# Kernel optimization log

Measured on AMD Instinct MI355X. Metric: run time of the kernel, lower is better.

## Reference

```python
import jax, jax.numpy as jnp
import numpy as np

N = 50000
IN_C, HID_C, CLS_C = 512, 256, 128
E = 800000


def setup_inputs() -> dict:
    key = jax.random.key(0)
    k1, k2, k3, k4, k5, k6 = jax.random.split(key, 6)
    x = jax.random.normal(k1, (N, IN_C), dtype=jnp.float32)
    edge_index = jax.random.randint(k2, (2, E), 0, N, dtype=jnp.int64)
    # GCNConv params (glorot weights, zero bias as in PyG init)
    W1 = jax.random.normal(k3, (IN_C, HID_C), dtype=jnp.float32) * (1.0 / np.sqrt(IN_C))
    b1 = jnp.zeros((HID_C,), dtype=jnp.float32)
    W2 = jax.random.normal(k4, (HID_C, CLS_C), dtype=jnp.float32) * (1.0 / np.sqrt(HID_C))
    b2 = jnp.zeros((CLS_C,), dtype=jnp.float32)
    return {"x": x, "W1": W1, "b1": b1, "W2": W2, "b2": b2, "edge_index": edge_index}


def _norm_edges(edge_index, n):
    # PyG GCNConv: add self-loops, symmetric normalization deg^-1/2
    loops = jnp.arange(n, dtype=edge_index.dtype)
    src = jnp.concatenate([edge_index[0], loops])
    dst = jnp.concatenate([edge_index[1], loops])
    ones = jnp.ones_like(src, dtype=jnp.float32)
    deg = jax.ops.segment_sum(ones, dst, num_segments=n)
    dinv = jnp.where(deg > 0, jax.lax.rsqrt(deg), 0.0)
    norm = dinv[src] * dinv[dst]  # [E+N]
    return src, dst, norm


def _gcn_conv(x, W, b, src, dst, norm, n):
    h = x @ W  # project first (out_channels < in_channels)
    msg = h[src] * norm[:, None]  # gather + scale, [E+N, C]
    out = jax.ops.segment_sum(msg, dst, num_segments=n)  # scatter-add
    return out + b


def reference(x, W1, b1, W2, b2, edge_index):
    n = x.shape[0]
    src, dst, norm = _norm_edges(edge_index, n)
    h = jax.nn.relu(_gcn_conv(x, W1, b1, src, dst, norm, n))
    # dropout p=0.5 is a no-op in eval mode
    out = _gcn_conv(h, W2, b2, src, dst, norm, n)
    return jax.nn.sigmoid(out)
```

## Files before the change

### kernel.cpp

```cpp
#include <hip/hip_runtime.h>

typedef __attribute__((ext_vector_type(8))) short bf16x8;
typedef __attribute__((ext_vector_type(4))) float f32x4;
typedef unsigned short u16;
typedef unsigned int u32;
typedef __attribute__((address_space(1))) const u32 gu32;
typedef __attribute__((address_space(3))) u32 lu32;

__device__ __forceinline__ float bf2f(u16 u) {
  union { u32 i; float f; } c; c.i = ((u32)u) << 16; return c.f;
}
__device__ __forceinline__ u16 f2bf(float f) {
  union { float f; u32 i; } c; c.f = f;
  u32 u = c.i;
  u32 r = (u + 0x7FFFu + ((u >> 16) & 1u)) >> 16;
  return (u16)r;
}

__device__ __forceinline__ void gld16(const void* g, void* l) {
  __builtin_amdgcn_global_load_lds((gu32*)g, (lu32*)l, 16, 0, 0);
}


__global__ void k_count(const int* __restrict__ ei, int* deg, int E) {
  int e = blockIdx.x * 256 + threadIdx.x;
  if (e < E) atomicAdd(&deg[ei[E + e]], 1);
}

__global__ void k_blocksum(const int* __restrict__ deg, int* bsum, int n) {
  __shared__ int s[256];
  int t = threadIdx.x;
  int i = blockIdx.x * 256 + t;
  s[t] = (i < n) ? deg[i] : 0;
  __syncthreads();
  for (int o = 128; o > 0; o >>= 1) {
    if (t < o) s[t] += s[t + o];
    __syncthreads();
  }
  if (t == 0) bsum[blockIdx.x] = s[0];
}

__global__ void k_scanb(const int* __restrict__ bsum, int* bofs, int nb) {
  __shared__ int s[256];
  int t = threadIdx.x;
  int v = (t < nb) ? bsum[t] : 0;
  s[t] = v;
  __syncthreads();
  for (int o = 1; o < 256; o <<= 1) {
    int x = (t >= o) ? s[t - o] : 0;
    __syncthreads();
    s[t] += x;
    __syncthreads();
  }
  bofs[t] = s[t] - v;
}

__global__ void k_rowptr(const int* __restrict__ deg, const int* __restrict__ bofs,
                         int* rowptr, int* cursor, float* dinv, int n) {
  __shared__ int s[256];
  int t = threadIdx.x;
  int i = blockIdx.x * 256 + t;
  int v = (i < n) ? deg[i] : 0;
  s[t] = v;
  __syncthreads();
  for (int o = 1; o < 256; o <<= 1) {
    int x = (t >= o) ? s[t - o] : 0;
    __syncthreads();
    s[t] += x;
    __syncthreads();
  }
  int excl = s[t] - v + bofs[blockIdx.x];
  if (i < n) {
    rowptr[i] = excl;
    cursor[i] = excl;
    dinv[i] = rsqrtf((float)(v + 1));
    if (i == n - 1) rowptr[n] = excl + v;
  }
}

__global__ void k_fill(const int* __restrict__ ei, int* cursor,
                       const float* __restrict__ dinv, int2* colw, int E) {
  int e = blockIdx.x * 256 + threadIdx.x;
  if (e >= E) return;
  int s = ei[e];
  int d = ei[E + e];
  int pos = atomicAdd(&cursor[d], 1);
  colw[pos] = make_int2(s, __float_as_int(dinv[s]));
}

__global__ void k_twt2(const float* __restrict__ W1, u16* __restrict__ W1t,
                       const float* __restrict__ W2, u16* __restrict__ W2t) {
  int i = blockIdx.x * 256 + threadIdx.x;
  if (i < 512 * 256) {
    int k = i >> 8, n = i & 255;
    W1t[n * 512 + k] = f2bf(W1[i]);
  } else {
    int j = i - 512 * 256;
    if (j < 256 * 128) {
      int k = j >> 7, n = j & 127;
      W2t[n * 256 + k] = f2bf(W2[j]);
    }
  }
}


template <bool AF32, int K, int BM, int MAXB>
__launch_bounds__(256, MAXB)
__global__ void gemm_kernel(const void* __restrict__ Ap, const u16* __restrict__ Bt,
                            u16* __restrict__ C, int M, int ldc) {
  constexpr int NT = K / 32;
  constexpr int ABYTES = BM * 32 * (AF32 ? 4 : 2);
  constexpr int AU16 = ABYTES / 2;
  constexpr int NJA = ABYTES / 4096;
  constexpr int S = NJA + 2;
  constexpr int WROWS = BM / 2;
  constexpr int FI = WROWS / 16;
  __shared__ u16 As_[2][AU16];
  __shared__ u16 Bs_[2][4096];

  const int tid = threadIdx.x;
  const int lane = tid & 63;
  const int wid = tid >> 6;
  const int wr = wid >> 1, wc = wid & 1;
  const long brow = (long)blockIdx.x * BM;
  const long bcol = (long)blockIdx.y * 128;

  const char* agp[NJA];
  char* alp[NJA];
#pragma unroll
  for (int j = 0; j < NJA; ++j) {
    int idx = j * 256 + tid;
    int row, u;
    if constexpr (AF32) { row = idx >> 3; u = (idx & 7) ^ (row & 7); }
    else                { row = idx >> 2; u = (idx & 3) ^ (row & 3); }
    long grow = brow + row; if (grow > (long)M - 1) grow = M - 1;
    agp[j] = (const char*)Ap + (grow * (long)K) * (AF32 ? 4 : 2) + u * 16;
    alp[j] = (char*)&As_[0][0] + idx * 16;
  }
  const u16* bgp[2];
  u16* blp[2];
#pragma unroll
  for (int j = 0; j < 2; ++j) {
    int idx = j * 256 + tid;
    int row = idx >> 2;
    int u = (idx & 3) ^ (row & 3);
    bgp[j] = Bt + (bcol + row) * (long)K + u * 8;
    blp[j] = &Bs_[0][idx * 8];
  }

  auto stage = [&](int kt, int buf) {
#pragma unroll
    for (int j = 0; j < NJA; ++j)
      gld16(agp[j] + kt * 32 * (AF32 ? 4 : 2), alp[j] + buf * ABYTES);
#pragma unroll
    for (int j = 0; j < 2; ++j) gld16(bgp[j] + kt * 32, blp[j] + buf * 4096);
  };

  f32x4 acc[FI][4];
#pragma unroll
  for (int i = 0; i < FI; i++)
#pragma unroll
    for (int j = 0; j < 4; j++) acc[i][j] = (f32x4){0.f, 0.f, 0.f, 0.f};

  stage(0, 0);
  int cur = 0;
  for (int kt = 0; kt < NT; ++kt) {
    if (kt + 1 < NT) {
      stage(kt + 1, cur ^ 1);
      asm volatile("s_waitcnt vmcnt(%0)" :: "n"(S) : "memory");
    } else {
      asm volatile("s_waitcnt vmcnt(0)" ::: "memory");
    }
    __builtin_amdgcn_s_barrier();
    __builtin_amdgcn_sched_barrier(0);

    bf16x8 af[FI], bfq[4];
#pragma unroll
    for (int i = 0; i < FI; i++) {
      const int row = wr * WROWS + i * 16 + (lane & 15);
      if constexpr (AF32) {
        const float* bp = (const float*)&As_[cur][0] + row * 32;
        const int s = row & 7;
        const int u0 = (lane >> 4) * 2;
        float4 x0 = *(const float4*)(bp + (u0 ^ s) * 4);
        float4 x1 = *(const float4*)(bp + ((u0 + 1) ^ s) * 4);
        union { u32 w[4]; bf16x8 v; } cv;
        asm("v_cvt_pk_bf16_f32 %0, %1, %2" : "=v"(cv.w[0]) : "v"(x0.x), "v"(x0.y));
        asm("v_cvt_pk_bf16_f32 %0, %1, %2" : "=v"(cv.w[1]) : "v"(x0.z), "v"(x0.w));
        asm("v_cvt_pk_bf16_f32 %0, %1, %2" : "=v"(cv.w[2]) : "v"(x1.x), "v"(x1.y));
        asm("v_cvt_pk_bf16_f32 %0, %1, %2" : "=v"(cv.w[3]) : "v"(x1.z), "v"(x1.w));
        af[i] = cv.v;
      } else {
        const int u = (lane >> 4) ^ (row & 3);
        af[i] = *(const bf16x8*)&As_[cur][row * 32 + u * 8];
      }
    }
#pragma unroll
    for (int j = 0; j < 4; j++) {
      const int row = wc * 64 + j * 16 + (lane & 15);
      const int u = (lane >> 4) ^ (row & 3);
      bfq[j] = *(const bf16x8*)&Bs_[cur][row * 32 + u * 8];
    }
#pragma unroll
    for (int i = 0; i < FI; i++)
#pragma unroll
      for (int j = 0; j < 4; j++)
        acc[i][j] = __builtin_amdgcn_mfma_f32_16x16x32_bf16(af[i], bfq[j], acc[i][j], 0, 0, 0);

    __builtin_amdgcn_sched_barrier(0);
    __builtin_amdgcn_s_barrier();
    cur ^= 1;
  }

#pragma unroll
  for (int i = 0; i < FI; i++) {
    const long r0 = brow + wr * WROWS + i * 16 + ((lane >> 4) * 4);
#pragma unroll
    for (int j = 0; j < 4; j++) {
      const long cc = bcol + wc * 64 + j * 16 + (lane & 15);
#pragma unroll
      for (int q = 0; q < 4; q++) {
        long r = r0 + q;
        if (r < M) C[r * (long)ldc + cc] = f2bf(acc[i][j][q]);
      }
    }
  }
}


__device__ __forceinline__ float sigmoidf_(float x) { return 1.f / (1.f + __expf(-x)); }

__launch_bounds__(256)
__global__ void agg1(const u16* __restrict__ h0, const int* __restrict__ rowptr,
                     const int2* __restrict__ colw, const float* __restrict__ dinv,
                     const float* __restrict__ b1, u16* __restrict__ h, int n) {
  const int wid = threadIdx.x >> 6, lane = threadIdx.x & 63;
  const int node = blockIdx.x * 4 + wid;
  if (node >= n) return;
  const float di = dinv[node];
  ushort4 sv = ((const ushort4*)(h0 + (size_t)node * 256))[lane];
  float a0 = di * bf2f(sv.x), a1 = di * bf2f(sv.y), a2 = di * bf2f(sv.z), a3 = di * bf2f(sv.w);
  int e = rowptr[node];
  const int r1 = rowptr[node + 1];
  for (; e + 8 <= r1; e += 8) {
    int2 c[8];
#pragma unroll
    for (int q = 0; q < 8; ++q) c[q] = colw[e + q];
    ushort4 v[8];
#pragma unroll
    for (int q = 0; q < 8; ++q)
      v[q] = ((const ushort4*)(h0 + (size_t)c[q].x * 256))[lane];
#pragma unroll
    for (int q = 0; q < 8; ++q) {
      float wv = __int_as_float(c[q].y);
      a0 += wv * bf2f(v[q].x); a1 += wv * bf2f(v[q].y);
      a2 += wv * bf2f(v[q].z); a3 += wv * bf2f(v[q].w);
    }
  }
  for (; e < r1; ++e) {
    int2 c = colw[e];
    float wv = __int_as_float(c.y);
    ushort4 v = ((const ushort4*)(h0 + (size_t)c.x * 256))[lane];
    a0 += wv * bf2f(v.x); a1 += wv * bf2f(v.y); a2 += wv * bf2f(v.z); a3 += wv * bf2f(v.w);
  }
  float4 bb = ((const float4*)b1)[lane];
  a0 = a0 * di + bb.x; a1 = a1 * di + bb.y; a2 = a2 * di + bb.z; a3 = a3 * di + bb.w;
  a0 = fmaxf(a0, 0.f); a1 = fmaxf(a1, 0.f); a2 = fmaxf(a2, 0.f); a3 = fmaxf(a3, 0.f);
  ushort4 o; o.x = f2bf(a0); o.y = f2bf(a1); o.z = f2bf(a2); o.w = f2bf(a3);
  ((ushort4*)(h + (size_t)node * 256))[lane] = o;
}

__launch_bounds__(256)
__global__ void agg2(const u16* __restrict__ h2, const int* __restrict__ rowptr,
                     const int2* __restrict__ colw, const float* __restrict__ dinv,
                     const float* __restrict__ b2, float* __restrict__ out, int n) {
  const int wid = threadIdx.x >> 6, lane = threadIdx.x & 63;
  const int node = blockIdx.x * 4 + wid;
  if (node >= n) return;
  const float di = dinv[node];
  ushort2 sv = ((const ushort2*)(h2 + (size_t)node * 128))[lane];
  float a0 = di * bf2f(sv.x), a1 = di * bf2f(sv.y);
  int e = rowptr[node];
  const int r1 = rowptr[node + 1];
  for (; e + 8 <= r1; e += 8) {
    int2 c[8];
#pragma unroll
    for (int q = 0; q < 8; ++q) c[q] = colw[e + q];
    ushort2 v[8];
#pragma unroll
    for (int q = 0; q < 8; ++q)
      v[q] = ((const ushort2*)(h2 + (size_t)c[q].x * 128))[lane];
#pragma unroll
    for (int q = 0; q < 8; ++q) {
      float wv = __int_as_float(c[q].y);
      a0 += wv * bf2f(v[q].x); a1 += wv * bf2f(v[q].y);
    }
  }
  for (; e < r1; ++e) {
    int2 c = colw[e];
    float wv = __int_as_float(c.y);
    ushort2 v = ((const ushort2*)(h2 + (size_t)c.x * 128))[lane];
    a0 += wv * bf2f(v.x); a1 += wv * bf2f(v.y);
  }
  float2 bb = ((const float2*)b2)[lane];
  float2 o;
  o.x = sigmoidf_(a0 * di + bb.x);
  o.y = sigmoidf_(a1 * di + bb.y);
  ((float2*)(out + (size_t)node * 128))[lane] = o;
}


extern "C" void kernel_launch(void* const* d_in, const int* in_sizes, int n_in,
                              void* d_out, int out_size, void* d_ws, size_t ws_size,
                              hipStream_t stream) {
  const float* x  = (const float*)d_in[0];
  const float* W1 = (const float*)d_in[1];
  const float* b1 = (const float*)d_in[2];
  const float* W2 = (const float*)d_in[3];
  const float* b2 = (const float*)d_in[4];
  const int*   ei = (const int*)d_in[5];

  const int N = in_sizes[0] / 512;
  const int E = in_sizes[5] / 2;
  const int Mpad = (N + 127) & ~127;
  float* outp = (float*)d_out;

  char* w = (char*)d_ws;
  size_t off = 0;
  auto take = [&](size_t bytes) -> void* {
    void* p = w + off;
    off = (off + bytes + 255) & ~(size_t)255;
    return p;
  };
  u16*   h0     = (u16*)take((size_t)Mpad * 256 * 2);
  u16*   hb     = (u16*)take((size_t)Mpad * 256 * 2);
  u16*   h2     = (u16*)take((size_t)Mpad * 128 * 2);
  u16*   W1t    = (u16*)take(256 * 512 * 2);
  u16*   W2t    = (u16*)take(128 * 256 * 2);
  int*   deg    = (int*)take((size_t)N * 4);
  float* dinv   = (float*)take((size_t)N * 4);
  int*   rowptr = (int*)take((size_t)(N + 1) * 4);
  int*   cursor = (int*)take((size_t)N * 4);
  int2*  colw   = (int2*)take((size_t)E * 8);
  int*   bsum   = (int*)take(256 * 4);
  int*   bofs   = (int*)take(256 * 4);
  (void)ws_size; (void)n_in; (void)out_size;

  const int nb = (N + 255) / 256;
  const int eb = (E + 255) / 256;

  hipMemsetAsync(deg, 0, (size_t)N * 4, stream);
  k_count<<<eb, 256, 0, stream>>>(ei, deg, E);
  k_blocksum<<<nb, 256, 0, stream>>>(deg, bsum, N);
  k_scanb<<<1, 256, 0, stream>>>(bsum, bofs, nb);
  k_rowptr<<<nb, 256, 0, stream>>>(deg, bofs, rowptr, cursor, dinv, N);
  k_fill<<<eb, 256, 0, stream>>>(ei, cursor, dinv, colw, E);
  k_twt2<<<(512 * 256 + 256 * 128 + 255) / 256, 256, 0, stream>>>(W1, W1t, W2, W2t);

  dim3 g1(Mpad / 128, 2);
  gemm_kernel<true, 512, 128, 3><<<g1, 256, 0, stream>>>((const void*)x, W1t, h0, N, 256);
  agg1<<<(N + 3) / 4, 256, 0, stream>>>(h0, rowptr, colw, dinv, b1, hb, N);
  dim3 g2(Mpad / 64, 1);
  gemm_kernel<false, 256, 64, 4><<<g2, 256, 0, stream>>>((const void*)hb, W2t, h2, Mpad, 128);
  agg2<<<(N + 3) / 4, 256, 0, stream>>>(h2, rowptr, colw, dinv, b2, outp, N);
}
```

Before: 253.7 us.

## Rewrite GEMMs to preload full B slab in LDS and stream A via registers

Replaces the double-buffered LDS-tiled GEMM with a 1024-thread kernel that loads the whole B column slab (K x 128) into shared memory once. Each wave then streams its own 16 rows of A directly from global memory into registers with a two-deep prefetch, so the main loop has no barriers. This removes per-k-step barrier synchronisation and A staging through LDS. In exchange it uses a large LDS footprint (128 KB for the first GEMM), which limits occupancy to one block per CU. Loads of A rows are also strided and less coalesced, and each block now does less MFMA work per B fetch.

```diff
diff --git a/kernel.cpp b/kernel.cpp
--- a/kernel.cpp
+++ b/kernel.cpp
@@ -104,125 +104,90 @@
 }
 
 
-template <bool AF32, int K, int BM, int MAXB>
-__launch_bounds__(256, MAXB)
-__global__ void gemm_kernel(const void* __restrict__ Ap, const u16* __restrict__ Bt,
-                            u16* __restrict__ C, int M, int ldc) {
+template <bool AF32, int K, int COLS>
+__launch_bounds__(1024)
+__global__ void gemm3(const void* __restrict__ Ap, const u16* __restrict__ Bt,
+                      u16* __restrict__ C, int M, int ldc) {
   constexpr int NT = K / 32;
-  constexpr int ABYTES = BM * 32 * (AF32 ? 4 : 2);
-  constexpr int AU16 = ABYTES / 2;
-  constexpr int NJA = ABYTES / 4096;
-  constexpr int S = NJA + 2;
-  constexpr int WROWS = BM / 2;
-  constexpr int FI = WROWS / 16;
-  __shared__ u16 As_[2][AU16];
-  __shared__ u16 Bs_[2][4096];
+  constexpr int SLABU = COLS * 4;
+  constexpr int NB = (COLS * K / 8) / 1024;
+  constexpr int NJ = COLS / 16;
+  __shared__ __align__(16) u16 Bs[NT][COLS * 32];
 
   const int tid = threadIdx.x;
   const int lane = tid & 63;
-  const int wid = tid >> 6;
-  const int wr = wid >> 1, wc = wid & 1;
-  const long brow = (long)blockIdx.x * BM;
-  const long bcol = (long)blockIdx.y * 128;
-
-  const char* agp[NJA];
-  char* alp[NJA];
-#pragma unroll
-  for (int j = 0; j < NJA; ++j) {
-    int idx = j * 256 + tid;
-    int row, u;
-    if constexpr (AF32) { row = idx >> 3; u = (idx & 7) ^ (row & 7); }
-    else                { row = idx >> 2; u = (idx & 3) ^ (row & 3); }
-    long grow = brow + row; if (grow > (long)M - 1) grow = M - 1;
-    agp[j] = (const char*)Ap + (grow * (long)K) * (AF32 ? 4 : 2) + u * 16;
-    alp[j] = (char*)&As_[0][0] + idx * 16;
-  }
-  const u16* bgp[2];
-  u16* blp[2];
-#pragma unroll
-  for (int j = 0; j < 2; ++j) {
-    int idx = j * 256 + tid;
-    int row = idx >> 2;
-    int u = (idx & 3) ^ (row & 3);
-    bgp[j] = Bt + (bcol + row) * (long)K + u * 8;
-    blp[j] = &Bs_[0][idx * 8];
-  }
-
-  auto stage = [&](int kt, int buf) {
-#pragma unroll
-    for (int j = 0; j < NJA; ++j)
-      gld16(agp[j] + kt * 32 * (AF32 ? 4 : 2), alp[j] + buf * ABYTES);
-#pragma unroll
-    for (int j = 0; j < 2; ++j) gld16(bgp[j] + kt * 32, blp[j] + buf * 4096);
+  const int w = tid >> 6;
+  const long brow = (long)blockIdx.y * 256;
+  const long bcol = (long)blockIdx.x * COLS;
+
+#pragma unroll
+  for (int j = 0; j < NB; ++j) {
+    int g = j * 1024 + tid;
+    int kt = g / SLABU;
+    int s = g - kt * SLABU;
+    int c = s >> 2;
+    int u = (s & 3) ^ (c & 3);
+    gld16(Bt + (bcol + c) * (long)K + kt * 32 + u * 8,
+          (char*)&Bs[0][0] + (size_t)g * 16);
+  }
+  __syncthreads();
+
+  long arow = brow + w * 16 + (lane & 15);
+  if (arow > (long)M - 1) arow = M - 1;
+  const char* ap = (const char*)Ap + (arow * (long)K + (lane >> 4) * 8) * (AF32 ? 4 : 2);
+  constexpr int AST = 32 * (AF32 ? 4 : 2);
+
+  f32x4 acc[NJ];
+#pragma unroll
+  for (int j = 0; j < NJ; ++j) acc[j] = (f32x4){0.f, 0.f, 0.f, 0.f};
+
+  float4 fa[2][2];
+  uint4 fb[2];
+  auto loadA = [&](int kt, int sl) {
+    if constexpr (AF32) {
+      fa[sl][0] = *(const float4*)(ap + (size_t)kt * AST);
+      fa[sl][1] = *(const float4*)(ap + (size_t)kt * AST + 16);
+    } else {
+      fb[sl] = *(const uint4*)(ap + (size_t)kt * AST);
+    }
   };
-
-  f32x4 acc[FI][4];
-#pragma unroll
-  for (int i = 0; i < FI; i++)
-#pragma unroll
-    for (int j = 0; j < 4; j++) acc[i][j] = (f32x4){0.f, 0.f, 0.f, 0.f};
-
-  stage(0, 0);
-  int cur = 0;
+  loadA(0, 0);
+  loadA(1, 1);
+
+#pragma unroll
   for (int kt = 0; kt < NT; ++kt) {
-    if (kt + 1 < NT) {
-      stage(kt + 1, cur ^ 1);
-      asm volatile("s_waitcnt vmcnt(%0)" :: "n"(S) : "memory");
+    const int sl = kt & 1;
+    bf16x8 af;
+    if constexpr (AF32) {
+      union { u32 wd[4]; bf16x8 v; } cv;
+      asm("v_cvt_pk_bf16_f32 %0, %1, %2" : "=v"(cv.wd[0]) : "v"(fa[sl][0].x), "v"(fa[sl][0].y));
+      asm("v_cvt_pk_bf16_f32 %0, %1, %2" : "=v"(cv.wd[1]) : "v"(fa[sl][0].z), "v"(fa[sl][0].w));
+      asm("v_cvt_pk_bf16_f32 %0, %1, %2" : "=v"(cv.wd[2]) : "v"(fa[sl][1].x), "v"(fa[sl][1].y));
+      asm("v_cvt_pk_bf16_f32 %0, %1, %2" : "=v"(cv.wd[3]) : "v"(fa[sl][1].z), "v"(fa[sl][1].w));
+      af = cv.v;
     } else {
-      asm volatile("s_waitcnt vmcnt(0)" ::: "memory");
-    }
-    __builtin_amdgcn_s_barrier();
-    __builtin_amdgcn_sched_barrier(0);
-
-    bf16x8 af[FI], bfq[4];
-#pragma unroll
-    for (int i = 0; i < FI; i++) {
-      const int row = wr * WROWS + i * 16 + (lane & 15);
-      if constexpr (AF32) {
-        const float* bp = (const float*)&As_[cur][0] + row * 32;
-        const int s = row & 7;
-        const int u0 = (lane >> 4) * 2;
-        float4 x0 = *(const float4*)(bp + (u0 ^ s) * 4);
-        float4 x1 = *(const float4*)(bp + ((u0 + 1) ^ s) * 4);
-        union { u32 w[4]; bf16x8 v; } cv;
-        asm("v_cvt_pk_bf16_f32 %0, %1, %2" : "=v"(cv.w[0]) : "v"(x0.x), "v"(x0.y));
-        asm("v_cvt_pk_bf16_f32 %0, %1, %2" : "=v"(cv.w[1]) : "v"(x0.z), "v"(x0.w));
-        asm("v_cvt_pk_bf16_f32 %0, %1, %2" : "=v"(cv.w[2]) : "v"(x1.x), "v"(x1.y));
-        asm("v_cvt_pk_bf16_f32 %0, %1, %2" : "=v"(cv.w[3]) : "v"(x1.z), "v"(x1.w));
-        af[i] = cv.v;
-      } else {
-        const int u = (lane >> 4) ^ (row & 3);
-        af[i] = *(const bf16x8*)&As_[cur][row * 32 + u * 8];
-      }
-    }
-#pragma unroll
-    for (int j = 0; j < 4; j++) {
-      const int row = wc * 64 + j * 16 + (lane & 15);
+      union { uint4 q; bf16x8 v; } cv2;
+      cv2.q = fb[sl];
+      af = cv2.v;
+    }
+    if (kt + 2 < NT) loadA(kt + 2, sl);
+#pragma unroll
+    for (int j = 0; j < NJ; ++j) {
+      const int row = j * 16 + (lane & 15);
       const int u = (lane >> 4) ^ (row & 3);
-      bfq[j] = *(const bf16x8*)&Bs_[cur][row * 32 + u * 8];
-    }
-#pragma unroll
-    for (int i = 0; i < FI; i++)
-#pragma unroll
-      for (int j = 0; j < 4; j++)
-        acc[i][j] = __builtin_amdgcn_mfma_f32_16x16x32_bf16(af[i], bfq[j], acc[i][j], 0, 0, 0);
-
-    __builtin_amdgcn_sched_barrier(0);
-    __builtin_amdgcn_s_barrier();
-    cur ^= 1;
-  }
-
-#pragma unroll
-  for (int i = 0; i < FI; i++) {
-    const long r0 = brow + wr * WROWS + i * 16 + ((lane >> 4) * 4);
-#pragma unroll
-    for (int j = 0; j < 4; j++) {
-      const long cc = bcol + wc * 64 + j * 16 + (lane & 15);
-#pragma unroll
-      for (int q = 0; q < 4; q++) {
-        long r = r0 + q;
-        if (r < M) C[r * (long)ldc + cc] = f2bf(acc[i][j][q]);
-      }
+      bf16x8 bq = *(const bf16x8*)&Bs[kt][row * 32 + u * 8];
+      acc[j] = __builtin_amdgcn_mfma_f32_16x16x32_bf16(af, bq, acc[j], 0, 0, 0);
+    }
+  }
+
+#pragma unroll
+  for (int j = 0; j < NJ; ++j) {
+    const long cc = bcol + j * 16 + (lane & 15);
+    const long r0 = brow + w * 16 + ((lane >> 4) * 4);
+#pragma unroll
+    for (int q = 0; q < 4; ++q) {
+      long r = r0 + q;
+      if (r < M) C[r * (long)ldc + cc] = f2bf(acc[j][q]);
     }
   }
 }
@@ -357,10 +322,11 @@
   k_fill<<<eb, 256, 0, stream>>>(ei, cursor, dinv, colw, E);
   k_twt2<<<(512 * 256 + 256 * 128 + 255) / 256, 256, 0, stream>>>(W1, W1t, W2, W2t);
 
-  dim3 g1(Mpad / 128, 2);
-  gemm_kernel<true, 512, 128, 3><<<g1, 256, 0, stream>>>((const void*)x, W1t, h0, N, 256);
+  const int rb = (N + 255) / 256;
+  dim3 g1(2, rb);
+  gemm3<true, 512, 128><<<g1, 1024, 0, stream>>>((const void*)x, W1t, h0, N, 256);
   agg1<<<(N + 3) / 4, 256, 0, stream>>>(h0, rowptr, colw, dinv, b1, hb, N);
-  dim3 g2(Mpad / 64, 1);
-  gemm_kernel<false, 256, 64, 4><<<g2, 256, 0, stream>>>((const void*)hb, W2t, h2, Mpad, 128);
+  dim3 g2(1, rb);
+  gemm3<false, 256, 128><<<g2, 1024, 0, stream>>>((const void*)hb, W2t, h2, N, 128);
   agg2<<<(N + 3) / 4, 256, 0, stream>>>(h2, rowptr, colw, dinv, b2, outp, N);
 }
```

Measured after the change: 253.8 us. No clear change (+0.0%).
